# Kernel optimization log

Measured on AMD Instinct MI355X. Metric: run time of the kernel, lower is better.

Reference implementation:

```python
import jax, jax.numpy as jnp
import numpy as np

# Per-feature MLP topology from NAM._get_topology: 1->32->64->128->64->32->16->1
DIMS = [1, 32, 64, 128, 64, 32, 16, 1]
N_LAYERS = len(DIMS) - 1  # 7 linear layers
BATCH, DIM = 2048, 256


def setup_inputs() -> dict:
    key = jax.random.key(0)
    inp = {"x": jax.random.normal(jax.random.fold_in(key, 0), (BATCH, DIM), dtype=jnp.float32)}
    # Batched parameters: stack the `dim` independent tiny MLPs along a leading axis.
    # torch.nn.Linear default init: U(-1/sqrt(fan_in), 1/sqrt(fan_in)) for W and b.
    for l in range(N_LAYERS):
        fi, fo = DIMS[l], DIMS[l + 1]
        kw, kb = jax.random.split(jax.random.fold_in(key, l + 1))
        bound = 1.0 / np.sqrt(fi)
        inp[f"W{l}"] = jax.random.uniform(kw, (DIM, fi, fo), jnp.float32, -bound, bound)
        inp[f"b{l}"] = jax.random.uniform(kb, (DIM, fo), jnp.float32, -bound, bound)
    return inp


def reference(x, W0, b0, W1, b1, W2, b2, W3, b3, W4, b4, W5, b5, W6, b6):
    Ws = [W0, W1, W2, W3, W4, W5, W6]
    bs = [b0, b1, b2, b3, b4, b5, b6]
    # h: [batch, dim, feat] — all `dim` tiny MLPs run as one batched GEMM per layer
    h = x[:, :, None]
    for l in range(N_LAYERS):
        h = jnp.einsum('bdi,dio->bdo', h, Ws[l]) + bs[l][None, :, :]
        if l < N_LAYERS - 1:
            h = jax.nn.relu(h)
    # funcs_sum = sum over features of each per-feature scalar output -> [batch, 1]
    return jnp.sum(h, axis=1)
```

## Files before the change

### kernel.cpp

```cpp
#include <hip/hip_runtime.h>

#define BATCH 2048
#define DIM   256

typedef _Float16 half8 __attribute__((ext_vector_type(8)));
typedef __attribute__((ext_vector_type(4))) float f32x4;

#define NTILES 41
#define TILE_HALVES 512

#define P_W0 0
#define P_B0 32
#define P_W6 64
#define P_B1 80
#define P_B2 144
#define P_B3 272
#define P_B4 336
#define P_B5 368
#define P_B6 384
#define P_TOT 385

struct Frag { half8 k0, k1, k2, k3; };

__device__ __forceinline__ half8 relu_pack(f32x4 e, f32x4 o) {
  half8 r;
#pragma unroll
  for (int j = 0; j < 4; ++j) {
    r[j]     = (_Float16)fmaxf(e[j], 0.0f);
    r[4 + j] = (_Float16)fmaxf(o[j], 0.0f);
  }
  return r;
}

template <int KT>
__device__ __forceinline__ f32x4 chain(const _Float16* __restrict__ tb,
                                       const Frag& a, f32x4 c) {
  c = __builtin_amdgcn_mfma_f32_16x16x32_f16(*(const half8*)tb, a.k0, c, 0, 0, 0);
  if constexpr (KT > 1)
    c = __builtin_amdgcn_mfma_f32_16x16x32_f16(*(const half8*)(tb + TILE_HALVES),
                                               a.k1, c, 0, 0, 0);
  if constexpr (KT > 2) {
    c = __builtin_amdgcn_mfma_f32_16x16x32_f16(
        *(const half8*)(tb + 2 * TILE_HALVES), a.k2, c, 0, 0, 0);
    c = __builtin_amdgcn_mfma_f32_16x16x32_f16(
        *(const half8*)(tb + 3 * TILE_HALVES), a.k3, c, 0, 0, 0);
  }
  return c;
}

template <int KT, int TBASE, int PB>
__device__ __forceinline__ void ntp_pair(
    const _Float16* __restrict__ packs, const float* __restrict__ pl, int lane,
    int q, const Frag& a0, const Frag& a1, const Frag& a2, const Frag& a3,
    half8& r0, half8& r1, half8& r2, half8& r3) {
  const f32x4 bias0 = *(const f32x4*)(pl + PB + (q << 2));
  const f32x4 bias1 = *(const f32x4*)(pl + PB + 16 + (q << 2));
  const _Float16* tb0 = packs + (size_t)TBASE * TILE_HALVES + lane * 8;
  const _Float16* tb1 = tb0 + (size_t)KT * TILE_HALVES;
  const f32x4 c00 = chain<KT>(tb0, a0, bias0);
  const f32x4 c01 = chain<KT>(tb0, a1, bias0);
  const f32x4 c02 = chain<KT>(tb0, a2, bias0);
  const f32x4 c03 = chain<KT>(tb0, a3, bias0);
  const f32x4 c10 = chain<KT>(tb1, a0, bias1);
  const f32x4 c11 = chain<KT>(tb1, a1, bias1);
  const f32x4 c12 = chain<KT>(tb1, a2, bias1);
  const f32x4 c13 = chain<KT>(tb1, a3, bias1);
  r0 = relu_pack(c00, c10);
  r1 = relu_pack(c01, c11);
  r2 = relu_pack(c02, c12);
  r3 = relu_pack(c03, c13);
}

template <int FI, int FO, int LBASE, int PBIAS>
__device__ __forceinline__ void layerX(
    const _Float16* __restrict__ packs, const float* __restrict__ pl, int lane,
    int q, const Frag& a0, const Frag& a1, const Frag& a2, const Frag& a3,
    Frag& o0, Frag& o1, Frag& o2, Frag& o3) {
  constexpr int KT = FI / 32, NTP = FO / 32;
  ntp_pair<KT, LBASE + 0 * 2 * KT, PBIAS + 0 * 32>(
      packs, pl, lane, q, a0, a1, a2, a3, o0.k0, o1.k0, o2.k0, o3.k0);
  if constexpr (NTP > 1)
    ntp_pair<KT, LBASE + 1 * 2 * KT, PBIAS + 1 * 32>(
        packs, pl, lane, q, a0, a1, a2, a3, o0.k1, o1.k1, o2.k1, o3.k1);
  if constexpr (NTP > 2) {
    ntp_pair<KT, LBASE + 2 * 2 * KT, PBIAS + 2 * 32>(
        packs, pl, lane, q, a0, a1, a2, a3, o0.k2, o1.k2, o2.k2, o3.k2);
    ntp_pair<KT, LBASE + 3 * 2 * KT, PBIAS + 3 * 32>(
        packs, pl, lane, q, a0, a1, a2, a3, o0.k3, o1.k3, o2.k3, o3.k3);
  }
}

__global__ __launch_bounds__(512, 2) void mlp_fused(
    const float* __restrict__ x,
    const float* __restrict__ W0, const float* __restrict__ b0,
    const float* __restrict__ W1, const float* __restrict__ b1,
    const float* __restrict__ W2, const float* __restrict__ b2,
    const float* __restrict__ W3, const float* __restrict__ b3,
    const float* __restrict__ W4, const float* __restrict__ b4,
    const float* __restrict__ W5, const float* __restrict__ b5,
    const float* __restrict__ W6, const float* __restrict__ b6,
    float* __restrict__ partial) {
  const int t = threadIdx.x;
  const int lane = t & 63;
  const int wave = t >> 6;
  const int m = lane & 15, q = lane >> 4;
  const int d = blockIdx.x;
  const int halfb = blockIdx.y;

  __shared__ __align__(16) _Float16 packs[NTILES * TILE_HALVES];
  __shared__ __align__(16) float xs[1024];
  __shared__ __align__(16) float pl[P_TOT];

  for (int i = t; i < 1024; i += 512)
    xs[i] = x[(size_t)(halfb * 1024 + i) * DIM + d];

  for (int job = t; job < NTILES * 64; job += 512) {
    const int tile = job >> 6, jl = job & 63;
    const int jm = jl & 15, jq = jl >> 4;
    const float* W; int FI, FO, lt;
    if (tile < 4)       { W = W1; FI = 32;  FO = 64;  lt = tile; }
    else if (tile < 20) { W = W2; FI = 64;  FO = 128; lt = tile - 4; }
    else if (tile < 36) { W = W3; FI = 128; FO = 64;  lt = tile - 20; }
    else if (tile < 40) { W = W4; FI = 64;  FO = 32;  lt = tile - 36; }
    else                { W = W5; FI = 32;  FO = 16;  lt = 0; }
    const int KT = FI >> 5;
    const int mt = lt / KT, kt = lt - mt * KT;
    const float* Wp = W + (size_t)d * FI * FO + (size_t)kt * 32 * FO +
                      mt * 16 + jm;
    half8 hi;
#pragma unroll
    for (int j = 0; j < 8; ++j) {
      const int fi = 16 * (j >> 2) + 4 * jq + (j & 3);
      hi[j] = (_Float16)Wp[(size_t)fi * FO];
    }
    *(half8*)(packs + (size_t)tile * TILE_HALVES + jl * 8) = hi;
  }
  for (int i = t; i < P_TOT; i += 512) {
    float v;
    if (i < 32)       v = W0[d * 32 + i];
    else if (i < 64)  v = b0[d * 32 + i - 32];
    else if (i < 80)  v = W6[d * 16 + i - 64];
    else if (i < 144) v = b1[d * 64 + i - 80];
    else if (i < 272) v = b2[d * 128 + i - 144];
    else if (i < 336) v = b3[d * 64 + i - 272];
    else if (i < 368) v = b4[d * 32 + i - 336];
    else if (i < 384) v = b5[d * 16 + i - 368];
    else              v = b6[d];
    pl[i] = v;
  }

  __syncthreads();

  Frag pA0, pA1, pA2, pA3, pB0, pB1, pB2, pB3;

  for (int it = 0; it < 2; ++it) {
    asm volatile("" ::: "memory");

    const int row0 = halfb * 1024 + it * 512 + wave * 64;

    const f32x4 w0a = *(const f32x4*)(pl + P_W0 + 4 * q);
    const f32x4 w0b = *(const f32x4*)(pl + P_W0 + 16 + 4 * q);
    const f32x4 b0a = *(const f32x4*)(pl + P_B0 + 4 * q);
    const f32x4 b0b = *(const f32x4*)(pl + P_B0 + 16 + 4 * q);

    {
      const int xb = it * 512 + wave * 64 + m;
      const float xv0 = xs[xb];
      const float xv1 = xs[xb + 16];
      const float xv2 = xs[xb + 32];
      const float xv3 = xs[xb + 48];
      half8 h0, h1, h2, h3;
#pragma unroll
      for (int j = 0; j < 4; ++j) {
        h0[j]     = (_Float16)fmaxf(fmaf(xv0, w0a[j], b0a[j]), 0.0f);
        h0[4 + j] = (_Float16)fmaxf(fmaf(xv0, w0b[j], b0b[j]), 0.0f);
        h1[j]     = (_Float16)fmaxf(fmaf(xv1, w0a[j], b0a[j]), 0.0f);
        h1[4 + j] = (_Float16)fmaxf(fmaf(xv1, w0b[j], b0b[j]), 0.0f);
        h2[j]     = (_Float16)fmaxf(fmaf(xv2, w0a[j], b0a[j]), 0.0f);
        h2[4 + j] = (_Float16)fmaxf(fmaf(xv2, w0b[j], b0b[j]), 0.0f);
        h3[j]     = (_Float16)fmaxf(fmaf(xv3, w0a[j], b0a[j]), 0.0f);
        h3[4 + j] = (_Float16)fmaxf(fmaf(xv3, w0b[j], b0b[j]), 0.0f);
      }
      pA0.k0 = h0;
      pA1.k0 = h1;
      pA2.k0 = h2;
      pA3.k0 = h3;
    }

    layerX<32, 64, 0, P_B1>(packs, pl, lane, q,
                            pA0, pA1, pA2, pA3, pB0, pB1, pB2, pB3);
    layerX<64, 128, 4, P_B2>(packs, pl, lane, q,
                             pB0, pB1, pB2, pB3, pA0, pA1, pA2, pA3);
    layerX<128, 64, 20, P_B3>(packs, pl, lane, q,
                              pA0, pA1, pA2, pA3, pB0, pB1, pB2, pB3);
    layerX<64, 32, 36, P_B4>(packs, pl, lane, q,
                             pB0, pB1, pB2, pB3, pA0, pA1, pA2, pA3);

    const f32x4 bias5 = *(const f32x4*)(pl + P_B5 + 4 * q);
    const f32x4 w6v = *(const f32x4*)(pl + P_W6 + 4 * q);
    const float bias6 = pl[P_B6];
    const half8 wf5 =
        *(const half8*)(packs + (size_t)40 * TILE_HALVES + lane * 8);

    const f32x4 a50 = __builtin_amdgcn_mfma_f32_16x16x32_f16(
        wf5, pA0.k0, bias5, 0, 0, 0);
    const f32x4 a51 = __builtin_amdgcn_mfma_f32_16x16x32_f16(
        wf5, pA1.k0, bias5, 0, 0, 0);
    const f32x4 a52 = __builtin_amdgcn_mfma_f32_16x16x32_f16(
        wf5, pA2.k0, bias5, 0, 0, 0);
    const f32x4 a53 = __builtin_amdgcn_mfma_f32_16x16x32_f16(
        wf5, pA3.k0, bias5, 0, 0, 0);
    float v0 = 0.0f, v1 = 0.0f, v2 = 0.0f, v3 = 0.0f;
#pragma unroll
    for (int r = 0; r < 4; ++r) {
      v0 += fmaxf(a50[r], 0.0f) * w6v[r];
      v1 += fmaxf(a51[r], 0.0f) * w6v[r];
      v2 += fmaxf(a52[r], 0.0f) * w6v[r];
      v3 += fmaxf(a53[r], 0.0f) * w6v[r];
    }
    v0 += __shfl_xor(v0, 16);
    v0 += __shfl_xor(v0, 32);
    v1 += __shfl_xor(v1, 16);
    v1 += __shfl_xor(v1, 32);
    v2 += __shfl_xor(v2, 16);
    v2 += __shfl_xor(v2, 32);
    v3 += __shfl_xor(v3, 16);
    v3 += __shfl_xor(v3, 32);
    if (q == 0) {
      partial[(size_t)d * BATCH + row0 + m]      = v0 + bias6;
      partial[(size_t)d * BATCH + row0 + 16 + m] = v1 + bias6;
      partial[(size_t)d * BATCH + row0 + 32 + m] = v2 + bias6;
      partial[(size_t)d * BATCH + row0 + 48 + m] = v3 + bias6;
    }
  }
}

__global__ __launch_bounds__(256) void reduce_kernel(
    const float* __restrict__ partial, float* __restrict__ out) {
  const int b = blockIdx.x * blockDim.x + threadIdx.x;
  float s = 0.0f;
#pragma unroll 8
  for (int d = 0; d < DIM; ++d) s += partial[(size_t)d * BATCH + b];
  out[b] = s;
}

extern "C" void kernel_launch(void* const* d_in, const int* in_sizes, int n_in,
                              void* d_out, int out_size, void* d_ws, size_t ws_size,
                              hipStream_t stream) {
  const float* x = (const float*)d_in[0];
  const float* W[7];
  const float* B[7];
  for (int l = 0; l < 7; ++l) {
    W[l] = (const float*)d_in[1 + 2 * l];
    B[l] = (const float*)d_in[2 + 2 * l];
  }
  float* partial = (float*)d_ws;

  mlp_fused<<<dim3(DIM, 2), dim3(512), 0, stream>>>(
      x, W[0], B[0], W[1], B[1], W[2], B[2], W[3], B[3], W[4], B[4], W[5], B[5],
      W[6], B[6], partial);

  reduce_kernel<<<dim3(BATCH / 256), dim3(256), 0, stream>>>(partial,
                                                             (float*)d_out);
}
```

Before: 133.4 us.

## Split weight packing into separate kernel and process full batch per block

Moves the strided fp32-to-fp16 weight transpose/pack into its own pre-pass kernel that writes contiguous packed tiles to workspace. The main kernel then copies those tiles into LDS with vectorized loads, and each block now handles all 2048 rows for one feature instead of two blocks per feature each redoing the pack. This removes the duplicated strided weight gathers but adds a kernel launch and a global round trip, and halves the grid to 256 blocks, which may reduce occupancy and parallelism on a large GPU.

```diff
diff --git a/kernel.cpp b/kernel.cpp
--- a/kernel.cpp
+++ b/kernel.cpp
@@ -8,6 +8,7 @@
 
 #define NTILES 41
 #define TILE_HALVES 512
+#define JOBS (NTILES * 64)
 
 #define P_W0 0
 #define P_B0 32
@@ -19,6 +20,11 @@
 #define P_B5 368
 #define P_B6 384
 #define P_TOT 385
+#define P_STRIDE 416
+
+#define WS_PACKED 0
+#define WS_PARAMS (12 << 20)
+#define WS_PARTIAL (16 << 20)
 
 struct Frag { half8 k0, k1, k2, k3; };
 
@@ -90,8 +96,7 @@
   }
 }
 
-__global__ __launch_bounds__(512, 2) void mlp_fused(
-    const float* __restrict__ x,
+__global__ __launch_bounds__(512) void pack_weights(
     const float* __restrict__ W0, const float* __restrict__ b0,
     const float* __restrict__ W1, const float* __restrict__ b1,
     const float* __restrict__ W2, const float* __restrict__ b2,
@@ -99,22 +104,10 @@
     const float* __restrict__ W4, const float* __restrict__ b4,
     const float* __restrict__ W5, const float* __restrict__ b5,
     const float* __restrict__ W6, const float* __restrict__ b6,
-    float* __restrict__ partial) {
+    _Float16* __restrict__ packed, float* __restrict__ params) {
   const int t = threadIdx.x;
-  const int lane = t & 63;
-  const int wave = t >> 6;
-  const int m = lane & 15, q = lane >> 4;
   const int d = blockIdx.x;
-  const int halfb = blockIdx.y;
-
-  __shared__ __align__(16) _Float16 packs[NTILES * TILE_HALVES];
-  __shared__ __align__(16) float xs[1024];
-  __shared__ __align__(16) float pl[P_TOT];
-
-  for (int i = t; i < 1024; i += 512)
-    xs[i] = x[(size_t)(halfb * 1024 + i) * DIM + d];
-
-  for (int job = t; job < NTILES * 64; job += 512) {
+  for (int job = t; job < JOBS; job += 512) {
     const int tile = job >> 6, jl = job & 63;
     const int jm = jl & 15, jq = jl >> 4;
     const float* W; int FI, FO, lt;
@@ -133,7 +126,7 @@
       const int fi = 16 * (j >> 2) + 4 * jq + (j & 3);
       hi[j] = (_Float16)Wp[(size_t)fi * FO];
     }
-    *(half8*)(packs + (size_t)tile * TILE_HALVES + jl * 8) = hi;
+    *(half8*)(packed + (size_t)d * JOBS * 8 + (size_t)job * 8) = hi;
   }
   for (int i = t; i < P_TOT; i += 512) {
     float v;
@@ -146,17 +139,39 @@
     else if (i < 368) v = b4[d * 32 + i - 336];
     else if (i < 384) v = b5[d * 16 + i - 368];
     else              v = b6[d];
-    pl[i] = v;
-  }
+    params[(size_t)d * P_STRIDE + i] = v;
+  }
+}
+
+__global__ __launch_bounds__(512, 2) void mlp_fused(
+    const float* __restrict__ x, const _Float16* __restrict__ packed,
+    const float* __restrict__ params, float* __restrict__ partial) {
+  const int t = threadIdx.x;
+  const int lane = t & 63;
+  const int wave = t >> 6;
+  const int m = lane & 15, q = lane >> 4;
+  const int d = blockIdx.x;
+
+  __shared__ __align__(16) _Float16 packs[NTILES * TILE_HALVES];
+  __shared__ __align__(16) float xs[2048];
+  __shared__ __align__(16) float pl[P_TOT];
+
+  const _Float16* gp = packed + (size_t)d * JOBS * 8;
+  for (int i = t; i < JOBS; i += 512)
+    *(half8*)(packs + (size_t)i * 8) = *(const half8*)(gp + (size_t)i * 8);
+  const float* gpar = params + (size_t)d * P_STRIDE;
+  for (int i = t; i < P_TOT; i += 512) pl[i] = gpar[i];
+  for (int i = t; i < 2048; i += 512)
+    xs[i] = x[(size_t)i * DIM + d];
 
   __syncthreads();
 
   Frag pA0, pA1, pA2, pA3, pB0, pB1, pB2, pB3;
 
-  for (int it = 0; it < 2; ++it) {
+  for (int it = 0; it < 4; ++it) {
     asm volatile("" ::: "memory");
 
-    const int row0 = halfb * 1024 + it * 512 + wave * 64;
+    const int row0 = it * 512 + wave * 64;
 
     const f32x4 w0a = *(const f32x4*)(pl + P_W0 + 4 * q);
     const f32x4 w0b = *(const f32x4*)(pl + P_W0 + 16 + 4 * q);
@@ -164,7 +179,7 @@
     const f32x4 b0b = *(const f32x4*)(pl + P_B0 + 16 + 4 * q);
 
     {
-      const int xb = it * 512 + wave * 64 + m;
+      const int xb = row0 + m;
       const float xv0 = xs[xb];
       const float xv1 = xs[xb + 16];
       const float xv2 = xs[xb + 32];
@@ -254,11 +269,16 @@
     W[l] = (const float*)d_in[1 + 2 * l];
     B[l] = (const float*)d_in[2 + 2 * l];
   }
-  float* partial = (float*)d_ws;
-
-  mlp_fused<<<dim3(DIM, 2), dim3(512), 0, stream>>>(
-      x, W[0], B[0], W[1], B[1], W[2], B[2], W[3], B[3], W[4], B[4], W[5], B[5],
-      W[6], B[6], partial);
+  char* ws = (char*)d_ws;
+  _Float16* packed = (_Float16*)(ws + WS_PACKED);
+  float* params = (float*)(ws + WS_PARAMS);
+  float* partial = (float*)(ws + WS_PARTIAL);
+
+  pack_weights<<<dim3(DIM), dim3(512), 0, stream>>>(
+      W[0], B[0], W[1], B[1], W[2], B[2], W[3], B[3], W[4], B[4], W[5], B[5],
+      W[6], B[6], packed, params);
+
+  mlp_fused<<<dim3(DIM), dim3(512), 0, stream>>>(x, packed, params, partial);
 
   reduce_kernel<<<dim3(BATCH / 256), dim3(256), 0, stream>>>(partial,
                                                              (float*)d_out);
```

New measurement: 137.8 us. 1.03x slower.

## Fuse reduction into MLP kernel via cooperative grid sync, one block per feature

Applied to the files above, without the earlier changes.

Each block now handles all 2048 batch rows for its feature, so the per-feature weight packing is done once per feature instead of twice. The kernel is launched cooperatively and, after a grid-wide sync, every block reduces partial sums for 8 output rows, which removes the second kernel launch. The trade-offs are half as many blocks (256 on a large GPU), less parallelism, a costly grid barrier, and an opaque register offset added to keep shared-memory loads from being hoisted.

```diff
diff --git a/kernel.cpp b/kernel.cpp
--- a/kernel.cpp
+++ b/kernel.cpp
@@ -1,4 +1,7 @@
 #include <hip/hip_runtime.h>
+#include <hip/hip_cooperative_groups.h>
+
+namespace cg = cooperative_groups;
 
 #define BATCH 2048
 #define DIM   256
@@ -8,6 +11,7 @@
 
 #define NTILES 41
 #define TILE_HALVES 512
+#define JOBS (NTILES * 64)
 
 #define P_W0 0
 #define P_B0 32
@@ -99,22 +103,22 @@
     const float* __restrict__ W4, const float* __restrict__ b4,
     const float* __restrict__ W5, const float* __restrict__ b5,
     const float* __restrict__ W6, const float* __restrict__ b6,
-    float* __restrict__ partial) {
+    float* __restrict__ partial, float* __restrict__ out) {
   const int t = threadIdx.x;
   const int lane = t & 63;
   const int wave = t >> 6;
   const int m = lane & 15, q = lane >> 4;
   const int d = blockIdx.x;
-  const int halfb = blockIdx.y;
 
   __shared__ __align__(16) _Float16 packs[NTILES * TILE_HALVES];
-  __shared__ __align__(16) float xs[1024];
+  __shared__ __align__(16) float xs[2048];
   __shared__ __align__(16) float pl[P_TOT];
-
-  for (int i = t; i < 1024; i += 512)
-    xs[i] = x[(size_t)(halfb * 1024 + i) * DIM + d];
-
-  for (int job = t; job < NTILES * 64; job += 512) {
+  __shared__ __align__(16) float red[64][8];
+
+  for (int i = t; i < 2048; i += 512)
+    xs[i] = x[(size_t)i * DIM + d];
+
+  for (int job = t; job < JOBS; job += 512) {
     const int tile = job >> 6, jl = job & 63;
     const int jm = jl & 15, jq = jl >> 4;
     const float* W; int FI, FO, lt;
@@ -153,18 +157,21 @@
 
   Frag pA0, pA1, pA2, pA3, pB0, pB1, pB2, pB3;
 
-  for (int it = 0; it < 2; ++it) {
-    asm volatile("" ::: "memory");
-
-    const int row0 = halfb * 1024 + it * 512 + wave * 64;
-
-    const f32x4 w0a = *(const f32x4*)(pl + P_W0 + 4 * q);
-    const f32x4 w0b = *(const f32x4*)(pl + P_W0 + 16 + 4 * q);
-    const f32x4 b0a = *(const f32x4*)(pl + P_B0 + 4 * q);
-    const f32x4 b0b = *(const f32x4*)(pl + P_B0 + 16 + 4 * q);
+  int opq = 0;
+  for (int it = 0; it < 4; ++it) {
+    asm volatile("" : "+v"(opq));
+    const _Float16* pk = packs + opq;
+    const float* plq = pl + opq;
+
+    const int row0 = it * 512 + wave * 64;
+
+    const f32x4 w0a = *(const f32x4*)(plq + P_W0 + 4 * q);
+    const f32x4 w0b = *(const f32x4*)(plq + P_W0 + 16 + 4 * q);
+    const f32x4 b0a = *(const f32x4*)(plq + P_B0 + 4 * q);
+    const f32x4 b0b = *(const f32x4*)(plq + P_B0 + 16 + 4 * q);
 
     {
-      const int xb = it * 512 + wave * 64 + m;
+      const int xb = row0 + m;
       const float xv0 = xs[xb];
       const float xv1 = xs[xb + 16];
       const float xv2 = xs[xb + 32];
@@ -187,20 +194,19 @@
       pA3.k0 = h3;
     }
 
-    layerX<32, 64, 0, P_B1>(packs, pl, lane, q,
+    layerX<32, 64, 0, P_B1>(pk, plq, lane, q,
                             pA0, pA1, pA2, pA3, pB0, pB1, pB2, pB3);
-    layerX<64, 128, 4, P_B2>(packs, pl, lane, q,
+    layerX<64, 128, 4, P_B2>(pk, plq, lane, q,
                              pB0, pB1, pB2, pB3, pA0, pA1, pA2, pA3);
-    layerX<128, 64, 20, P_B3>(packs, pl, lane, q,
+    layerX<128, 64, 20, P_B3>(pk, plq, lane, q,
                               pA0, pA1, pA2, pA3, pB0, pB1, pB2, pB3);
-    layerX<64, 32, 36, P_B4>(packs, pl, lane, q,
+    layerX<64, 32, 36, P_B4>(pk, plq, lane, q,
                              pB0, pB1, pB2, pB3, pA0, pA1, pA2, pA3);
 
-    const f32x4 bias5 = *(const f32x4*)(pl + P_B5 + 4 * q);
-    const f32x4 w6v = *(const f32x4*)(pl + P_W6 + 4 * q);
-    const float bias6 = pl[P_B6];
-    const half8 wf5 =
-        *(const half8*)(packs + (size_t)40 * TILE_HALVES + lane * 8);
+    const f32x4 bias5 = *(const f32x4*)(plq + P_B5 + 4 * q);
+    const f32x4 w6v = *(const f32x4*)(plq + P_W6 + 4 * q);
+    const float bias6 = plq[P_B6];
+    const half8 wf5 = *(const half8*)(pk + (size_t)40 * TILE_HALVES + lane * 8);
 
     const f32x4 a50 = __builtin_amdgcn_mfma_f32_16x16x32_f16(
         wf5, pA0.k0, bias5, 0, 0, 0);
@@ -233,33 +239,49 @@
       partial[(size_t)d * BATCH + row0 + 48 + m] = v3 + bias6;
     }
   }
-}
-
-__global__ __launch_bounds__(256) void reduce_kernel(
-    const float* __restrict__ partial, float* __restrict__ out) {
-  const int b = blockIdx.x * blockDim.x + threadIdx.x;
+
+  __threadfence();
+  cg::this_grid().sync();
+
+  const int dg = t >> 3, bl = t & 7;
+  const int bout = d * 8 + bl;
   float s = 0.0f;
-#pragma unroll 8
-  for (int d = 0; d < DIM; ++d) s += partial[(size_t)d * BATCH + b];
-  out[b] = s;
+#pragma unroll
+  for (int k = 0; k < 4; ++k)
+    s += partial[(size_t)(dg * 4 + k) * BATCH + bout];
+  red[dg][bl] = s;
+  __syncthreads();
+  if (t < 8) {
+    float acc = 0.0f;
+    for (int j = 0; j < 64; ++j) acc += red[j][t];
+    out[d * 8 + t] = acc;
+  }
 }
 
 extern "C" void kernel_launch(void* const* d_in, const int* in_sizes, int n_in,
                               void* d_out, int out_size, void* d_ws, size_t ws_size,
                               hipStream_t stream) {
   const float* x = (const float*)d_in[0];
-  const float* W[7];
-  const float* B[7];
-  for (int l = 0; l < 7; ++l) {
-    W[l] = (const float*)d_in[1 + 2 * l];
-    B[l] = (const float*)d_in[2 + 2 * l];
-  }
+  const float* W0 = (const float*)d_in[1];
+  const float* B0 = (const float*)d_in[2];
+  const float* W1 = (const float*)d_in[3];
+  const float* B1 = (const float*)d_in[4];
+  const float* W2 = (const float*)d_in[5];
+  const float* B2 = (const float*)d_in[6];
+  const float* W3 = (const float*)d_in[7];
+  const float* B3 = (const float*)d_in[8];
+  const float* W4 = (const float*)d_in[9];
+  const float* B4 = (const float*)d_in[10];
+  const float* W5 = (const float*)d_in[11];
+  const float* B5 = (const float*)d_in[12];
+  const float* W6 = (const float*)d_in[13];
+  const float* B6 = (const float*)d_in[14];
   float* partial = (float*)d_ws;
-
-  mlp_fused<<<dim3(DIM, 2), dim3(512), 0, stream>>>(
-      x, W[0], B[0], W[1], B[1], W[2], B[2], W[3], B[3], W[4], B[4], W[5], B[5],
-      W[6], B[6], partial);
-
-  reduce_kernel<<<dim3(BATCH / 256), dim3(256), 0, stream>>>(partial,
-                                                             (float*)d_out);
-}
+  float* out = (float*)d_out;
+
+  void* args[] = {&x,  &W0, &B0, &W1, &B1, &W2, &B2, &W3, &B3,
+                  &W4, &B4, &W5, &B5, &W6, &B6, &partial, &out};
+
+  hipLaunchCooperativeKernel((const void*)mlp_fused, dim3(DIM), dim3(512),
+                             args, 0, stream);
+}
```

New measurement: 210.0 us. 1.57x slower.
